# Performance work log

Hardware: AMD Instinct MI355X
Metric: run time of the kernel (lower is better)

The kernel has to match this reference:

```python
import jax, jax.numpy as jnp
import numpy as np

B, L, H, A = 2, 1024, 768, 12          # batch, doc_len, hidden, attn heads
E, M, P = 24, 8, 552                   # entities/doc, mentions/entity, entity pairs/doc
EMB, BLK, NL = 768, 64, 97             # emb_size, block_size, num relation labels
OFFSET = 1                             # [CLS] offset


def setup_inputs() -> dict:
    key = jax.random.key(0)
    ks = jax.random.split(key, 16)
    w = lambda k, shape: (jax.random.normal(k, shape, jnp.float32) * 0.02)
    return {
        'sequence_output': jax.random.normal(ks[0], (B, L, H), jnp.float32),
        'attention': jax.random.uniform(ks[1], (B, A, L, L), jnp.float32),
        'mention_mask': jnp.ones((B, E, M), jnp.float32),
        'Wh': w(ks[2], (2 * H, EMB)),  'bh': jnp.zeros((EMB,), jnp.float32),
        'Wt': w(ks[3], (2 * H, EMB)),  'bt': jnp.zeros((EMB,), jnp.float32),
        'Wh2': w(ks[4], (3 * H, EMB)), 'bh2': jnp.zeros((EMB,), jnp.float32),
        'Wt2': w(ks[5], (3 * H, EMB)), 'bt2': jnp.zeros((EMB,), jnp.float32),
        'W2': w(ks[6], (EMB * BLK, H)), 'b2': jnp.zeros((H,), jnp.float32),
        'Wb': w(ks[7], (EMB * BLK, NL)), 'bb': jnp.zeros((NL,), jnp.float32),
        'mention_idx': jax.random.randint(ks[8], (B, E, M), 0, L - OFFSET),
        'hts': jax.random.randint(ks[9], (B, P, 2), 0, E),
    }


def _block_bilinear(a, b):
    # grouped (block) bilinear: [N, EMB] x [N, EMB] -> [N, EMB*BLK]
    b1 = a.reshape(-1, EMB // BLK, BLK)
    b2 = b.reshape(-1, EMB // BLK, BLK)
    return jnp.einsum('nkb,nkc->nkbc', b1, b2).reshape(-1, EMB * BLK)


def reference(sequence_output, attention, mention_mask,
              Wh, bh, Wt, bt, Wh2, bh2, Wt2, bt2, W2, b2, Wb, bb,
              mention_idx, hts):
    bidx = jnp.arange(B)[:, None, None]
    pos = mention_idx + OFFSET                              # [B,E,M]

    # --- get_hrt: ragged mention gather + logsumexp / mean pooling ---
    ment_emb = sequence_output[bidx, pos]                   # [B,E,M,H]
    mm = mention_mask[..., None]
    x = jnp.where(mm > 0, ment_emb, -1e30)
    mx = x.max(axis=2, keepdims=True)
    ent_emb = (mx + jnp.log(jnp.sum(jnp.exp(x - mx), axis=2, keepdims=True))).squeeze(2)  # [B,E,H]

    ment_att = attention[bidx, :, pos]                      # [B,E,M,A,L]
    cnt = jnp.clip(mention_mask.sum(-1), 1.0)[:, :, None, None]
    ent_att = (ment_att * mention_mask[..., None, None]).sum(2) / cnt  # [B,E,A,L]

    bidx2 = jnp.arange(B)[:, None]
    hs = ent_emb[bidx2, hts[..., 0]]                        # [B,P,H]
    ts = ent_emb[bidx2, hts[..., 1]]
    h_att = ent_att[bidx2, hts[..., 0]]                     # [B,P,A,L]
    t_att = ent_att[bidx2, hts[..., 1]]
    ht_att = (h_att * t_att).mean(2)                        # [B,P,L]
    ht_att = ht_att / (ht_att.sum(-1, keepdims=True) + 1e-30)
    rs = jnp.einsum('bpl,blh->bph', ht_att, sequence_output)  # localized context

    hs = hs.reshape(-1, H); ts = ts.reshape(-1, H); rs = rs.reshape(-1, H)

    # --- forward_rel: extractors + grouped block-bilinear scoring ---
    hs1 = jnp.tanh(jnp.concatenate([hs, rs], -1) @ Wh + bh)
    ts1 = jnp.tanh(jnp.concatenate([ts, rs], -1) @ Wt + bt)
    hts_feat = _block_bilinear(hs1, ts1) @ W2 + b2          # [N,H]
    hs2 = jnp.tanh(jnp.concatenate([hs1, rs, hts_feat], -1) @ Wh2 + bh2)
    ts2 = jnp.tanh(jnp.concatenate([ts1, rs, hts_feat], -1) @ Wt2 + bt2)
    logits = _block_bilinear(hs2, ts2) @ Wb + bb            # [N,NL]
    return logits
```

## Files before the change

### kernel.cpp

```cpp
#include <hip/hip_runtime.h>
#include <hip/hip_bf16.h>

#define B_ 2
#define L_ 1024
#define H_ 768
#define A_ 12
#define E_ 24
#define M_ 8
#define P_ 552
#define EMB_ 768
#define BLK_ 64
#define NBLK_ 12
#define NL_ 97
#define NP_ (B_*P_)
#define KTOT_ 49152
#define TP_ 8
#define LC_ 128
#define NC_ (L_/LC_)

typedef float f32x4 __attribute__((ext_vector_type(4)));
typedef _Float16 f16x8 __attribute__((ext_vector_type(8)));

static __device__ __forceinline__ unsigned short f2h(float f){
    _Float16 h = (_Float16)f;
    unsigned short u; __builtin_memcpy(&u, &h, 2); return u;
}

__global__ void k_ent_emb(const float* __restrict__ seq, const float* __restrict__ mask,
                          const int* __restrict__ midx, float* __restrict__ ent_emb)
{
    int be = blockIdx.x;
    int b = be / E_;
    int h = threadIdx.x;
    float v[M_];
    float mx = -1e30f;
    #pragma unroll
    for (int m = 0; m < M_; ++m) {
        float w = mask[be*M_ + m];
        int p = midx[be*M_ + m] + 1;
        float x = (w > 0.f) ? seq[(b*L_ + p)*H_ + h] : -1e30f;
        v[m] = x; mx = fmaxf(mx, x);
    }
    float s = 0.f;
    #pragma unroll
    for (int m = 0; m < M_; ++m) s += expf(v[m] - mx);
    ent_emb[be*H_ + h] = mx + logf(s);
}

__global__ void k_ent_att(const float* __restrict__ att, const float* __restrict__ mask,
                          const int* __restrict__ midx, float* __restrict__ ent_att)
{
    int bea = blockIdx.x;
    int a = bea % A_;
    int be = bea / A_;
    int b = be / E_;
    float cnt = 0.f;
    #pragma unroll
    for (int m = 0; m < M_; ++m) cnt += mask[be*M_ + m];
    cnt = fmaxf(cnt, 1.f);
    float inv = 1.f / cnt;
    for (int l = threadIdx.x; l < L_; l += blockDim.x) {
        float acc = 0.f;
        #pragma unroll
        for (int m = 0; m < M_; ++m) {
            float w = mask[be*M_ + m];
            if (w > 0.f) {
                int p = midx[be*M_ + m] + 1;
                acc += w * att[((size_t)(b*A_ + a)*L_ + p)*L_ + l];
            }
        }
        ent_att[(size_t)(be*A_ + a)*L_ + l] = acc * inv;
    }
}

__global__ void k_ht_att(const float* __restrict__ ent_att, const int* __restrict__ hts,
                         float* __restrict__ ht_att)
{
    int bp = blockIdx.x;
    int b = bp / P_;
    int he = hts[bp*2 + 0];
    int te = hts[bp*2 + 1];
    const float* ha = ent_att + (size_t)(b*E_ + he)*A_*L_;
    const float* ta = ent_att + (size_t)(b*E_ + te)*A_*L_;
    __shared__ float red[256];
    float lsum = 0.f;
    for (int l = threadIdx.x; l < L_; l += 256) {
        float q = 0.f;
        #pragma unroll
        for (int a = 0; a < A_; ++a) q += ha[a*L_ + l] * ta[a*L_ + l];
        q *= (1.f / A_);
        ht_att[(size_t)bp*L_ + l] = q;
        lsum += q;
    }
    red[threadIdx.x] = lsum;
    __syncthreads();
    for (int s = 128; s > 0; s >>= 1) {
        if (threadIdx.x < s) red[threadIdx.x] += red[threadIdx.x + s];
        __syncthreads();
    }
    float scale = 1.f / (red[0] + 1e-30f);
    for (int l = threadIdx.x; l < L_; l += 256)
        ht_att[(size_t)bp*L_ + l] *= scale;
}

__global__ void k_rs_part(const float* __restrict__ seq, const float* __restrict__ ht_att,
                          float* __restrict__ rspart)
{
    int blk = blockIdx.x;
    int chunk = blockIdx.y;
    int b = blk / (P_/TP_);
    int p0 = (blk % (P_/TP_)) * TP_;
    const float* sq = seq + ((size_t)b*L_ + (size_t)chunk*LC_)*H_;
    const float* wb = ht_att + (size_t)(b*P_ + p0)*L_ + chunk*LC_;
    float acc[TP_][3];
    #pragma unroll
    for (int t = 0; t < TP_; ++t)
        #pragma unroll
        for (int c = 0; c < 3; ++c) acc[t][c] = 0.f;
    for (int l = 0; l < LC_; ++l) {
        float w[TP_];
        #pragma unroll
        for (int t = 0; t < TP_; ++t) w[t] = wb[(size_t)t*L_ + l];
        #pragma unroll
        for (int c = 0; c < 3; ++c) {
            float v = sq[(size_t)l*H_ + threadIdx.x + 256*c];
            #pragma unroll
            for (int t = 0; t < TP_; ++t) acc[t][c] += w[t]*v;
        }
    }
    #pragma unroll
    for (int t = 0; t < TP_; ++t)
        #pragma unroll
        for (int c = 0; c < 3; ++c)
            rspart[((size_t)chunk*NP_ + b*P_ + p0 + t)*H_ + threadIdx.x + 256*c] = acc[t][c];
}

__global__ void k_rs_reduce(const float* __restrict__ rspart, float* __restrict__ rs)
{
    int idx = blockIdx.x*256 + threadIdx.x;
    if (idx >= NP_*768/4) return;
    f32x4 s = {0.f,0.f,0.f,0.f};
    #pragma unroll
    for (int z = 0; z < NC_; ++z) s += *(const f32x4*)&rspart[(size_t)z*NP_*768 + (size_t)idx*4];
    *(f32x4*)&rs[(size_t)idx*4] = s;
}

__global__ void k_rs(const float* __restrict__ seq, const float* __restrict__ ht_att,
                     float* __restrict__ rs)
{
    int blk = blockIdx.x;
    int b = blk / (P_/TP_);
    int p0 = (blk % (P_/TP_)) * TP_;
    const float* sq = seq + (size_t)b*L_*H_;
    float acc[TP_][3];
    #pragma unroll
    for (int t = 0; t < TP_; ++t)
        #pragma unroll
        for (int c = 0; c < 3; ++c) acc[t][c] = 0.f;
    for (int l = 0; l < L_; ++l) {
        float w[TP_];
        #pragma unroll
        for (int t = 0; t < TP_; ++t) w[t] = ht_att[(size_t)(b*P_ + p0 + t)*L_ + l];
        #pragma unroll
        for (int c = 0; c < 3; ++c) {
            float v = sq[(size_t)l*H_ + threadIdx.x + 256*c];
            #pragma unroll
            for (int t = 0; t < TP_; ++t) acc[t][c] += w[t]*v;
        }
    }
    #pragma unroll
    for (int t = 0; t < TP_; ++t)
        #pragma unroll
        for (int c = 0; c < 3; ++c)
            rs[(size_t)(b*P_ + p0 + t)*H_ + threadIdx.x + 256*c] = acc[t][c];
}

__global__ void k_gather(const float* __restrict__ ent_emb, const int* __restrict__ hts,
                         float* __restrict__ hs, float* __restrict__ ts)
{
    int bp = blockIdx.x;
    int b = bp / P_;
    int he = hts[bp*2 + 0];
    int te = hts[bp*2 + 1];
    int h = threadIdx.x;
    hs[(size_t)bp*H_ + h] = ent_emb[(b*E_ + he)*H_ + h];
    ts[(size_t)bp*H_ + h] = ent_emb[(b*E_ + te)*H_ + h];
}

__global__ void k_gemm_reduce_tanh2(const float* __restrict__ gpA, const float* __restrict__ gpB,
                                    const float* __restrict__ biasA, const float* __restrict__ biasB,
                                    float* __restrict__ CA, float* __restrict__ CB, int nz)
{
    const float* Cpart = blockIdx.y ? gpB : gpA;
    const float* bias  = blockIdx.y ? biasB : biasA;
    float* C           = blockIdx.y ? CB : CA;
    int idx = blockIdx.x*256 + threadIdx.x;
    if (idx >= NP_*768/4) return;
    int c4 = (idx*4) % 768;
    f32x4 s = *(const f32x4*)&bias[c4];
    for (int z = 0; z < nz; ++z) s += *(const f32x4*)&Cpart[(size_t)z*NP_*768 + (size_t)idx*4];
    f32x4 r;
    #pragma unroll
    for (int j = 0; j < 4; ++j) r[j] = tanhf(s[j]);
    *(f32x4*)&C[(size_t)idx*4] = r;
}

template<int NPARTS, bool DOTANH>
__global__ void k_gemm_concat(const float* __restrict__ A0, const float* __restrict__ A1,
                              const float* __restrict__ A2, const float* __restrict__ W,
                              const float* __restrict__ bias, float* __restrict__ C,
                              int Mrows)
{
    const int BK = 16;
    __shared__ float As[BK][64];
    __shared__ float Bs[BK][64];
    int tid = threadIdx.x;
    int ty = tid >> 4, tx = tid & 15;
    int by = blockIdx.y, bx = blockIdx.x;
    float acc[4][4] = {};
    const int K = NPARTS * 768;
    for (int kk0 = 0; kk0 < K; kk0 += BK) {
        const float* Ap = (kk0 < 768) ? A0 : ((NPARTS >= 3 && kk0 >= 1536) ? A2 : A1);
        int klocal = kk0 % 768;
        {
            int idx = tid * 4;
            int r = idx >> 4;
            int k = idx & 15;
            int row = by*64 + r;
            float4 v = make_float4(0.f,0.f,0.f,0.f);
            if (row < Mrows) v = *(const float4*)(Ap + (size_t)row*768 + klocal + k);
            As[k+0][r] = v.x; As[k+1][r] = v.y; As[k+2][r] = v.z; As[k+3][r] = v.w;
        }
        {
            int idx = tid * 4;
            int k = idx >> 6;
            int c = idx & 63;
            *(float4*)&Bs[k][c] = *(const float4*)(W + (size_t)(kk0 + k)*768 + bx*64 + c);
        }
        __syncthreads();
        #pragma unroll
        for (int k = 0; k < BK; ++k) {
            float a4[4], b4[4];
            *(float4*)a4 = *(float4*)&As[k][ty*4];
            *(float4*)b4 = *(float4*)&Bs[k][tx*4];
            #pragma unroll
            for (int i = 0; i < 4; ++i)
                #pragma unroll
                for (int j = 0; j < 4; ++j) acc[i][j] += a4[i]*b4[j];
        }
        __syncthreads();
    }
    #pragma unroll
    for (int i = 0; i < 4; ++i) {
        int row = by*64 + ty*4 + i;
        if (row >= Mrows) continue;
        #pragma unroll
        for (int j = 0; j < 4; ++j) {
            int col = bx*64 + tx*4 + j;
            float v = acc[i][j] + bias[col];
            if (DOTANH) v = tanhf(v);
            C[(size_t)row*768 + col] = v;
        }
    }
}

__global__ void k_wt_f16(const float* __restrict__ in, unsigned short* __restrict__ out,
                         int K, int N, int Npad)
{
    __shared__ float t[64][65];
    int k0 = blockIdx.x*64, c0 = blockIdx.y*64;
    int tx = threadIdx.x & 63, ty = threadIdx.x >> 6;
    #pragma unroll
    for (int q = 0; q < 16; ++q) {
        int r = ty*16 + q;
        float v = 0.f;
        if (c0 + tx < N) v = in[(size_t)(k0 + r)*N + c0 + tx];
        t[r][tx] = v;
    }
    __syncthreads();
    #pragma unroll
    for (int q = 0; q < 16; ++q) {
        int col = ty*16 + q;
        if (c0 + col < Npad) out[(size_t)(c0+col)*K + k0 + tx] = f2h(t[tx][col]);
    }
}

__global__ void k_wt_f16x2(const float* __restrict__ in0, unsigned short* __restrict__ out0,
                           const float* __restrict__ in1, unsigned short* __restrict__ out1,
                           int K, int N, int Npad)
{
    const float* in = blockIdx.z ? in1 : in0;
    unsigned short* out = blockIdx.z ? out1 : out0;
    __shared__ float t[64][65];
    int k0 = blockIdx.x*64, c0 = blockIdx.y*64;
    int tx = threadIdx.x & 63, ty = threadIdx.x >> 6;
    #pragma unroll
    for (int q = 0; q < 16; ++q) {
        int r = ty*16 + q;
        float v = 0.f;
        if (c0 + tx < N) v = in[(size_t)(k0 + r)*N + c0 + tx];
        t[r][tx] = v;
    }
    __syncthreads();
    #pragma unroll
    for (int q = 0; q < 16; ++q) {
        int col = ty*16 + q;
        if (c0 + col < Npad) out[(size_t)(c0+col)*K + k0 + tx] = f2h(t[tx][col]);
    }
}

template<int NSTEP>
__launch_bounds__(256, 3)
__global__ void k_gemm_mfma2(const float* __restrict__ A0a, const float* __restrict__ A0b,
                             const float* __restrict__ A1, const float* __restrict__ A2,
                             const unsigned short* __restrict__ WTa, const unsigned short* __restrict__ WTb,
                             float* __restrict__ Cpa, float* __restrict__ Cpb,
                             int Mrows, int Ktot, int partdiv, int nzhalf)
{
    __shared__ _Float16 Ash[128][64];
    __shared__ _Float16 Bsh[128][64];
    int tid = threadIdx.x;
    int lane = tid & 63, wid = tid >> 6;
    int wr = (wid >> 1)*64, wc = (wid & 1)*64;
    int r16 = lane & 15, g = lane >> 4;
    int zz = blockIdx.z;
    int half = zz / nzhalf;
    int z = zz % nzhalf;
    const unsigned short* WT = half ? WTb : WTa;
    float* Cpart = half ? Cpb : Cpa;
    int part = z / partdiv, chunk = z % partdiv;
    int ka = chunk * (NSTEP*64);
    int kb = part*768 + ka;
    const float* A = (part == 0) ? (half ? A0b : A0a) : ((part == 1) ? A1 : A2);
    int c0 = blockIdx.x*128;
    int row0 = blockIdx.y*128;

    f32x4 acc[4][4];
    #pragma unroll
    for (int a = 0; a < 4; ++a)
        #pragma unroll
        for (int b = 0; b < 4; ++b) acc[a][b] = (f32x4){0.f,0.f,0.f,0.f};

    for (int s = 0; s < NSTEP; ++s) {
        __syncthreads();
        #pragma unroll
        for (int q = 0; q < 4; ++q) {
            int idx = q*256 + tid;
            int row = idx >> 3, ch = idx & 7;
            int grow = row0 + row; if (grow >= Mrows) grow = Mrows - 1;
            const float* p = &A[(size_t)grow*768 + ka + s*64 + ch*8];
            f32x4 a0 = *(const f32x4*)p;
            f32x4 a1 = *(const f32x4*)(p + 4);
            f16x8 h;
            h[0]=(_Float16)a0[0]; h[1]=(_Float16)a0[1]; h[2]=(_Float16)a0[2]; h[3]=(_Float16)a0[3];
            h[4]=(_Float16)a1[0]; h[5]=(_Float16)a1[1]; h[6]=(_Float16)a1[2]; h[7]=(_Float16)a1[3];
            *(f16x8*)&Ash[row][(ch ^ (row & 7))*8] = h;
        }
        #pragma unroll
        for (int q = 0; q < 4; ++q) {
            int idx = q*256 + tid;
            int col = idx >> 3, ch = idx & 7;
            *(f16x8*)&Bsh[col][(ch ^ (col & 7))*8] =
                *(const f16x8*)&WT[(size_t)(c0+col)*Ktot + kb + s*64 + ch*8];
        }
        __syncthreads();
        #pragma unroll
        for (int kk = 0; kk < 2; ++kk) {
            f16x8 bfr[4];
            #pragma unroll
            for (int ni = 0; ni < 4; ++ni)
                bfr[ni] = *(f16x8*)&Bsh[wc + ni*16 + r16][((kk*4 + g) ^ (r16 & 7))*8];
            #pragma unroll
            for (int mi = 0; mi < 4; ++mi) {
                f16x8 afr = *(f16x8*)&Ash[wr + mi*16 + r16][((kk*4 + g) ^ (r16 & 7))*8];
                #pragma unroll
                for (int ni = 0; ni < 4; ++ni)
                    acc[mi][ni] = __builtin_amdgcn_mfma_f32_16x16x32_f16(afr, bfr[ni], acc[mi][ni], 0, 0, 0);
            }
        }
    }

    #pragma unroll
    for (int mi = 0; mi < 4; ++mi)
      #pragma unroll
      for (int ni = 0; ni < 4; ++ni)
        #pragma unroll
        for (int r = 0; r < 4; ++r) {
            int row = row0 + wr + mi*16 + g*4 + r;
            if (row < Mrows)
                Cpart[((size_t)z*Mrows + row)*768 + c0 + wc + ni*16 + r16] = acc[mi][ni][r];
        }
}

template<int ILEN, bool SWZ>
__launch_bounds__(256, 3)
__global__ void k_bb_mfma(const float* __restrict__ U, const float* __restrict__ V,
                          const unsigned short* __restrict__ BT, float* __restrict__ Cpart,
                          int Mrows, int ldc)
{
    const int ISPLIT = 64 / ILEN;
    __shared__ unsigned short Ush[128][ILEN + 2];
    __shared__ _Float16 Bs[2][128][64];
    int tid = threadIdx.x;
    int lane = tid & 63, wid = tid >> 6;
    int wr = (wid >> 1)*64, wc = (wid & 1)*64;
    int r16 = lane & 15, g = lane >> 4;
    int bx = blockIdx.x, by = blockIdx.y, z = blockIdx.z;
    if (SWZ) {
        int h = bx + 6*by + 54*z;
        int x = h & 7, j = h >> 3;
        int p = x*9 + j/9;
        by = j % 9;
        bx = p % 6;
        z  = p / 6;
    }
    int kz = z / ISPLIT, si = z % ISPLIT;
    int ibeg = si * ILEN;
    int c0 = bx*128;
    int row0 = by*128;

    #pragma unroll
    for (int q = 0; q < (128*ILEN)/1024; ++q) {
        int idx = (q*256 + tid)*4;
        int r = idx / ILEN, c = idx % ILEN;
        int row = row0 + r; if (row >= Mrows) row = Mrows - 1;
        f32x4 v = *(const f32x4*)&U[(size_t)row*EMB_ + kz*64 + ibeg + c];
        Ush[r][c+0] = f2h(v[0]); Ush[r][c+1] = f2h(v[1]);
        Ush[r][c+2] = f2h(v[2]); Ush[r][c+3] = f2h(v[3]);
    }
    f16x8 vfh[2][4];
    #pragma unroll
    for (int kk = 0; kk < 2; ++kk)
      #pragma unroll
      for (int mi = 0; mi < 4; ++mi) {
        int row = row0 + wr + mi*16 + r16; if (row >= Mrows) row = Mrows - 1;
        const float* p = &V[(size_t)row*EMB_ + kz*64 + kk*32 + g*8];
        f16x8 t;
        #pragma unroll
        for (int e = 0; e < 8; ++e) t[e] = (_Float16)p[e];
        vfh[kk][mi] = t;
      }
    #pragma unroll
    for (int q = 0; q < 4; ++q) {
        int idx = q*256 + tid;
        int col = idx >> 3, ch = idx & 7;
        *(f16x8*)&Bs[0][col][(ch ^ (col & 7))*8] =
            *(const f16x8*)&BT[(size_t)(c0+col)*KTOT_ + (size_t)kz*4096 + (size_t)ibeg*64 + ch*8];
    }
    __syncthreads();

    f32x4 acc[4][4];
    #pragma unroll
    for (int a = 0; a < 4; ++a)
        #pragma unroll
        for (int b = 0; b < 4; ++b) acc[a][b] = (f32x4){0.f,0.f,0.f,0.f};

    f16x8 breg[4];
    for (int ii = 0; ii < ILEN; ++ii) {
        int cur = ii & 1, nxt = cur ^ 1;
        if (ii < ILEN-1) {
            #pragma unroll
            for (int q = 0; q < 4; ++q) {
                int idx = q*256 + tid;
                int col = idx >> 3, ch = idx & 7;
                breg[q] = *(const f16x8*)&BT[(size_t)(c0+col)*KTOT_ + (size_t)kz*4096
                                             + (size_t)(ibeg+ii+1)*64 + ch*8];
            }
        }
        f16x8 u8[4];
        #pragma unroll
        for (int mi = 0; mi < 4; ++mi) {
            unsigned short ub = Ush[wr + mi*16 + r16][ii];
            _Float16 uh; __builtin_memcpy(&uh, &ub, 2);
            #pragma unroll
            for (int e = 0; e < 8; ++e) u8[mi][e] = uh;
        }
        #pragma unroll
        for (int kk = 0; kk < 2; ++kk) {
            f16x8 bfr[4];
            #pragma unroll
            for (int ni = 0; ni < 4; ++ni) {
                int row = wc + ni*16 + r16;
                bfr[ni] = *(f16x8*)&Bs[cur][row][((kk*4 + g) ^ (r16 & 7))*8];
            }
            #pragma unroll
            for (int mi = 0; mi < 4; ++mi) {
                f16x8 afr = u8[mi] * vfh[kk][mi];
                #pragma unroll
                for (int ni = 0; ni < 4; ++ni)
                    acc[mi][ni] = __builtin_amdgcn_mfma_f32_16x16x32_f16(afr, bfr[ni], acc[mi][ni], 0, 0, 0);
            }
        }
        if (ii < ILEN-1) {
            #pragma unroll
            for (int q = 0; q < 4; ++q) {
                int idx = q*256 + tid;
                int col = idx >> 3, ch = idx & 7;
                *(f16x8*)&Bs[nxt][col][(ch ^ (col & 7))*8] = breg[q];
            }
        }
        __syncthreads();
    }

    #pragma unroll
    for (int mi = 0; mi < 4; ++mi)
      #pragma unroll
      for (int ni = 0; ni < 4; ++ni)
        #pragma unroll
        for (int r = 0; r < 4; ++r) {
            int row = row0 + wr + mi*16 + g*4 + r;
            if (row < Mrows)
                Cpart[((size_t)z*Mrows + row)*ldc + c0 + wc + ni*16 + r16] = acc[mi][ni][r];
        }
}

__global__ void k_reduce_feat(const float* __restrict__ part, const float* __restrict__ bias,
                              float* __restrict__ out)
{
    int idx = blockIdx.x*256 + threadIdx.x;
    if (idx >= (NP_*768)/4) return;
    int c4 = (idx*4) % 768;
    f32x4 s = *(const f32x4*)&bias[c4];
    #pragma unroll
    for (int z = 0; z < NBLK_; ++z) s += *(const f32x4*)&part[(size_t)z*NP_*768 + (size_t)idx*4];
    *(f32x4*)&out[(size_t)idx*4] = s;
}

__global__ void k_reduce_logits(const float* __restrict__ part, const float* __restrict__ bb,
                                float* __restrict__ out, int nz)
{
    int idx = blockIdx.x*256 + threadIdx.x;
    if (idx >= NP_*NL_) return;
    int n = idx / NL_, c = idx % NL_;
    float s = bb[c];
    for (int z = 0; z < nz; ++z) s += part[(size_t)z*NP_*128 + (size_t)n*128 + c];
    out[idx] = s;
}

template<bool GUARD, bool SPLITK>
__global__ void k_bbgemm(const float* __restrict__ U, const float* __restrict__ V,
                         const float* __restrict__ W, const float* __restrict__ bias,
                         float* __restrict__ C, int Mrows, int Ncols, int ldw, int ldc)
{
    __shared__ float Us[64][68];
    __shared__ float Vs[64][68];
    __shared__ float Bsh[16][64];
    int tid = threadIdx.x;
    int ty = tid >> 4, tx = tid & 15;
    int by = blockIdx.y, bx = blockIdx.x;
    int c0 = bx*64;
    float acc[4][4] = {};
    int kbeg = SPLITK ? blockIdx.z : 0;
    int kend = SPLITK ? blockIdx.z + 1 : NBLK_;
    for (int k = kbeg; k < kend; ++k) {
        #pragma unroll
        for (int e = 0; e < 4; ++e) {
            int idx = (e*256 + tid)*4;
            int r = idx >> 6, c = idx & 63;
            int row = by*64 + r;
            float4 u = make_float4(0.f,0.f,0.f,0.f), vv = make_float4(0.f,0.f,0.f,0.f);
            if (row < Mrows) {
                u  = *(const float4*)(U + (size_t)row*EMB_ + k*BLK_ + c);
                vv = *(const float4*)(V + (size_t)row*EMB_ + k*BLK_ + c);
            }
            *(float4*)&Us[r][c] = u;
            *(float4*)&Vs[r][c] = vv;
        }
        __syncthreads();
        for (int t = 0; t < 256; ++t) {
            int i = t >> 2;
            int jb = (t & 3) * 16;
            {
                int idx = tid * 4;
                int kk = idx >> 6, c = idx & 63;
                size_t wrow = (size_t)(k*256 + t)*16 + kk;
                if (GUARD) {
                    #pragma unroll
                    for (int q = 0; q < 4; ++q) {
                        int col = c0 + c + q;
                        Bsh[kk][c+q] = (col < Ncols) ? W[wrow*ldw + col] : 0.f;
                    }
                } else {
                    *(float4*)&Bsh[kk][c] = *(const float4*)(W + wrow*ldw + c0 + c);
                }
            }
            __syncthreads();
            float u[4];
            #pragma unroll
            for (int r = 0; r < 4; ++r) u[r] = Us[ty*4+r][i];
            #pragma unroll
            for (int kk = 0; kk < 16; ++kk) {
                float b4[4];
                *(float4*)b4 = *(float4*)&Bsh[kk][tx*4];
                #pragma unroll
                for (int r = 0; r < 4; ++r) {
                    float a = u[r] * Vs[ty*4+r][jb+kk];
                    #pragma unroll
                    for (int j = 0; j < 4; ++j) acc[r][j] += a*b4[j];
                }
            }
            __syncthreads();
        }
    }
    #pragma unroll
    for (int r = 0; r < 4; ++r) {
        int row = by*64 + ty*4 + r;
        if (row >= Mrows) continue;
        #pragma unroll
        for (int j = 0; j < 4; ++j) {
            int col = c0 + tx*4 + j;
            if (GUARD && col >= Ncols) continue;
            float v = acc[r][j];
            if (!SPLITK) v += bias[col];
            size_t out_idx = SPLITK ? ((size_t)(blockIdx.z*Mrows + row)*ldc + col)
                                    : ((size_t)row*ldc + col);
            C[out_idx] = v;
        }
    }
}

__global__ void k_logits_reduce_old(const float* __restrict__ part, const float* __restrict__ bb,
                                    float* __restrict__ out)
{
    int idx = blockIdx.x*256 + threadIdx.x;
    if (idx >= NP_*NL_) return;
    int col = idx % NL_;
    float s = bb[col];
    #pragma unroll
    for (int z = 0; z < NBLK_; ++z) s += part[(size_t)z*NP_*NL_ + idx];
    out[idx] = s;
}

extern "C" void kernel_launch(void* const* d_in, const int* in_sizes, int n_in,
                              void* d_out, int out_size, void* d_ws, size_t ws_size,
                              hipStream_t stream)
{
    (void)in_sizes; (void)n_in; (void)out_size;
    const float* seq  = (const float*)d_in[0];
    const float* att  = (const float*)d_in[1];
    const float* mask = (const float*)d_in[2];
    const float* Wh   = (const float*)d_in[3];
    const float* bh   = (const float*)d_in[4];
    const float* Wt   = (const float*)d_in[5];
    const float* bt   = (const float*)d_in[6];
    const float* Wh2  = (const float*)d_in[7];
    const float* bh2  = (const float*)d_in[8];
    const float* Wt2  = (const float*)d_in[9];
    const float* bt2  = (const float*)d_in[10];
    const float* W2   = (const float*)d_in[11];
    const float* b2   = (const float*)d_in[12];
    const float* Wb   = (const float*)d_in[13];
    const float* bb   = (const float*)d_in[14];
    const int* midx   = (const int*)d_in[15];
    const int* hts    = (const int*)d_in[16];
    float* out = (float*)d_out;
    float* ws  = (float*)d_ws;

    float* ent_emb = ws;
    float* ent_att = ent_emb + 36864;
    float* ht_att  = ent_att + 589824;
    float* rs      = ht_att + 1130496;
    float* hs      = rs   + 847872;
    float* ts      = hs   + 847872;
    float* hs1     = ts   + 847872;
    float* ts1     = hs1  + 847872;
    float* feat    = ts1  + 847872;
    float* hs2     = feat + 847872;
    float* ts2     = hs2  + 847872;
    float* featpart = ts2 + 847872;
    float* spare    = featpart + 10174464;
    unsigned short* w2t = (unsigned short*)(spare + 1695744);
    unsigned short* Rrgn = (unsigned short*)(spare + 1695744 + 18874368);
    const size_t need_bytes = (size_t)42430464 * 4;
    const bool use_mfma = (ws_size >= need_bytes);

    unsigned short* whT  = Rrgn;
    unsigned short* wtT  = Rrgn + 1179648;
    unsigned short* wh2T = Rrgn;
    unsigned short* wt2T = Rrgn + 1769472;
    unsigned short* wbt  = Rrgn;

    float* rspart  = featpart;
    float* gpA     = featpart;
    float* gpB     = featpart + 5087232;
    float* logpart = featpart;

    k_ent_emb<<<dim3(B_*E_), dim3(H_), 0, stream>>>(seq, mask, midx, ent_emb);
    k_ent_att<<<dim3(B_*E_*A_), dim3(256), 0, stream>>>(att, mask, midx, ent_att);
    k_ht_att<<<dim3(NP_), dim3(256), 0, stream>>>(ent_att, hts, ht_att);

    if (use_mfma) {
        k_rs_part<<<dim3(B_*(P_/TP_), NC_), dim3(256), 0, stream>>>(seq, ht_att, rspart);
        k_rs_reduce<<<dim3(828), dim3(256), 0, stream>>>(rspart, rs);
        k_gather<<<dim3(NP_), dim3(H_), 0, stream>>>(ent_emb, hts, hs, ts);

        k_wt_f16x2<<<dim3(1536/64, 768/64, 2), dim3(256), 0, stream>>>(Wh, whT, Wt, wtT, 1536, 768, 768);

        k_gemm_mfma2<4><<<dim3(6, 9, 12), dim3(256), 0, stream>>>(
            hs, ts, rs, rs, whT, wtT, gpA, gpB, NP_, 1536, 3, 6);
        k_gemm_reduce_tanh2<<<dim3(828, 2), dim3(256), 0, stream>>>(gpA, gpB, bh, bt, hs1, ts1, 6);

        k_wt_f16<<<dim3(KTOT_/64, 768/64), dim3(256), 0, stream>>>(W2, w2t, KTOT_, 768, 768);
        k_bb_mfma<64, true><<<dim3(6, 9, NBLK_), dim3(256), 0, stream>>>(hs1, ts1, w2t, featpart, NP_, 768);
        k_reduce_feat<<<dim3((NP_*768/4 + 255)/256), dim3(256), 0, stream>>>(featpart, b2, feat);

        k_wt_f16x2<<<dim3(2304/64, 768/64, 2), dim3(256), 0, stream>>>(Wh2, wh2T, Wt2, wt2T, 2304, 768, 768);

        k_gemm_mfma2<6><<<dim3(6, 9, 12), dim3(256), 0, stream>>>(
            hs1, ts1, rs, feat, wh2T, wt2T, gpA, gpB, NP_, 2304, 2, 6);
        k_gemm_reduce_tanh2<<<dim3(828, 2), dim3(256), 0, stream>>>(gpA, gpB, bh2, bt2, hs2, ts2, 6);

        k_wt_f16<<<dim3(KTOT_/64, 128/64), dim3(256), 0, stream>>>(Wb, wbt, KTOT_, NL_, 128);
        k_bb_mfma<16, false><<<dim3(1, 9, NBLK_*4), dim3(256), 0, stream>>>(hs2, ts2, wbt, logpart, NP_, 128);
        k_reduce_logits<<<dim3((NP_*NL_ + 255)/256), dim3(256), 0, stream>>>(logpart, bb, out, NBLK_*4);
    } else {
        k_rs<<<dim3(B_*(P_/TP_)), dim3(256), 0, stream>>>(seq, ht_att, rs);
        k_gather<<<dim3(NP_), dim3(H_), 0, stream>>>(ent_emb, hts, hs, ts);
        dim3 gg(12, (NP_+63)/64);
        k_gemm_concat<2, true><<<gg, dim3(256), 0, stream>>>(hs, rs, nullptr, Wh, bh, hs1, NP_);
        k_gemm_concat<2, true><<<gg, dim3(256), 0, stream>>>(ts, rs, nullptr, Wt, bt, ts1, NP_);
        float* lpart = featpart;
        k_bbgemm<false, false><<<gg, dim3(256), 0, stream>>>(hs1, ts1, W2, b2, feat, NP_, 768, 768, 768);
        k_gemm_concat<3, true><<<gg, dim3(256), 0, stream>>>(hs1, rs, feat, Wh2, bh2, hs2, NP_);
        k_gemm_concat<3, true><<<gg, dim3(256), 0, stream>>>(ts1, rs, feat, Wt2, bt2, ts2, NP_);
        k_bbgemm<true, true><<<dim3(2, (NP_+63)/64, NBLK_), dim3(256), 0, stream>>>(
            hs2, ts2, Wb, nullptr, lpart, NP_, NL_, NL_, NL_);
        k_logits_reduce_old<<<dim3((NP_*NL_ + 255)/256), dim3(256), 0, stream>>>(lpart, bb, out);
    }
}
```

Before: 392.9 us.

## Compute localized context with MFMA GEMM and fuse gather into extractor GEMM

Replaces the scalar FP32 rs_part kernel with an MFMA f16 GEMM over ht_att and a transposed f16 copy of sequence_output. The transpose is merged with the W2 conversion into one multi-task transpose kernel. The hs/ts gather kernel is removed: the first extractor GEMM indexes ent_emb directly through hts. This cuts launches and scalar FMA work, at the cost of f16 rounding of the attention weights and the sequence values in the rs computation.

Result: faster. 349.5 us (-11.0%).

```diff
diff --git a/kernel.cpp b/kernel.cpp
--- a/kernel.cpp
+++ b/kernel.cpp
@@ -15,8 +15,7 @@
 #define NP_ (B_*P_)
 #define KTOT_ 49152
 #define TP_ 8
-#define LC_ 128
-#define NC_ (L_/LC_)
+#define NC_ 8
 
 typedef float f32x4 __attribute__((ext_vector_type(4)));
 typedef _Float16 f16x8 __attribute__((ext_vector_type(8)));
@@ -103,36 +102,147 @@
         ht_att[(size_t)bp*L_ + l] *= scale;
 }
 
-__global__ void k_rs_part(const float* __restrict__ seq, const float* __restrict__ ht_att,
-                          float* __restrict__ rspart)
-{
-    int blk = blockIdx.x;
-    int chunk = blockIdx.y;
-    int b = blk / (P_/TP_);
-    int p0 = (blk % (P_/TP_)) * TP_;
-    const float* sq = seq + ((size_t)b*L_ + (size_t)chunk*LC_)*H_;
-    const float* wb = ht_att + (size_t)(b*P_ + p0)*L_ + chunk*LC_;
-    float acc[TP_][3];
-    #pragma unroll
-    for (int t = 0; t < TP_; ++t)
-        #pragma unroll
-        for (int c = 0; c < 3; ++c) acc[t][c] = 0.f;
-    for (int l = 0; l < LC_; ++l) {
-        float w[TP_];
-        #pragma unroll
-        for (int t = 0; t < TP_; ++t) w[t] = wb[(size_t)t*L_ + l];
-        #pragma unroll
-        for (int c = 0; c < 3; ++c) {
-            float v = sq[(size_t)l*H_ + threadIdx.x + 256*c];
-            #pragma unroll
-            for (int t = 0; t < TP_; ++t) acc[t][c] += w[t]*v;
-        }
-    }
-    #pragma unroll
-    for (int t = 0; t < TP_; ++t)
-        #pragma unroll
-        for (int c = 0; c < 3; ++c)
-            rspart[((size_t)chunk*NP_ + b*P_ + p0 + t)*H_ + threadIdx.x + 256*c] = acc[t][c];
+__global__ void k_wt_multi(const float* __restrict__ W2, unsigned short* __restrict__ w2t,
+                           const float* __restrict__ seq, unsigned short* __restrict__ seqT)
+{
+    int t = blockIdx.x;
+    const float* in; unsigned short* out; int K, N, kt, ct;
+    if (t < 9216)       { in = W2;              out = w2t;             K = KTOT_; N = 768; kt = t % 768; ct = t / 768; }
+    else if (t < 9408)  { t -= 9216; in = seq;                 out = seqT;              K = L_; N = 768; kt = t % 16; ct = t / 16; }
+    else                { t -= 9408; in = seq + (size_t)L_*H_; out = seqT + (size_t)768*L_; K = L_; N = 768; kt = t % 16; ct = t / 16; }
+    __shared__ float tl[64][65];
+    int k0 = kt*64, c0 = ct*64;
+    int tx = threadIdx.x & 63, ty = threadIdx.x >> 6;
+    #pragma unroll
+    for (int q = 0; q < 16; ++q) {
+        int r = ty*16 + q;
+        tl[r][tx] = in[(size_t)(k0 + r)*N + c0 + tx];
+    }
+    __syncthreads();
+    #pragma unroll
+    for (int q = 0; q < 16; ++q) {
+        int col = ty*16 + q;
+        out[(size_t)(c0+col)*K + k0 + tx] = f2h(tl[tx][col]);
+    }
+}
+
+__global__ void k_wt_f16(const float* __restrict__ in, unsigned short* __restrict__ out,
+                         int K, int N, int Npad)
+{
+    __shared__ float t[64][65];
+    int k0 = blockIdx.x*64, c0 = blockIdx.y*64;
+    int tx = threadIdx.x & 63, ty = threadIdx.x >> 6;
+    #pragma unroll
+    for (int q = 0; q < 16; ++q) {
+        int r = ty*16 + q;
+        float v = 0.f;
+        if (c0 + tx < N) v = in[(size_t)(k0 + r)*N + c0 + tx];
+        t[r][tx] = v;
+    }
+    __syncthreads();
+    #pragma unroll
+    for (int q = 0; q < 16; ++q) {
+        int col = ty*16 + q;
+        if (c0 + col < Npad) out[(size_t)(c0+col)*K + k0 + tx] = f2h(t[tx][col]);
+    }
+}
+
+__global__ void k_wt_f16x2(const float* __restrict__ in0, unsigned short* __restrict__ out0,
+                           const float* __restrict__ in1, unsigned short* __restrict__ out1,
+                           int K, int N, int Npad)
+{
+    const float* in = blockIdx.z ? in1 : in0;
+    unsigned short* out = blockIdx.z ? out1 : out0;
+    __shared__ float t[64][65];
+    int k0 = blockIdx.x*64, c0 = blockIdx.y*64;
+    int tx = threadIdx.x & 63, ty = threadIdx.x >> 6;
+    #pragma unroll
+    for (int q = 0; q < 16; ++q) {
+        int r = ty*16 + q;
+        float v = 0.f;
+        if (c0 + tx < N) v = in[(size_t)(k0 + r)*N + c0 + tx];
+        t[r][tx] = v;
+    }
+    __syncthreads();
+    #pragma unroll
+    for (int q = 0; q < 16; ++q) {
+        int col = ty*16 + q;
+        if (c0 + col < Npad) out[(size_t)(c0+col)*K + k0 + tx] = f2h(t[tx][col]);
+    }
+}
+
+__launch_bounds__(256, 3)
+__global__ void k_rs_mfma(const float* __restrict__ ht_att, const unsigned short* __restrict__ seqT,
+                          float* __restrict__ Cpart)
+{
+    __shared__ _Float16 Ash[128][64];
+    __shared__ _Float16 Bsh[128][64];
+    int tid = threadIdx.x;
+    int lane = tid & 63, wid = tid >> 6;
+    int wr = (wid >> 1)*64, wc = (wid & 1)*64;
+    int r16 = lane & 15, g = lane >> 4;
+    int z = blockIdx.z;
+    int b = z >> 3, kc = z & 7;
+    int c0 = blockIdx.x*128;
+    int row0 = blockIdx.y*128;
+    const float* At = ht_att + (size_t)b*P_*L_;
+    const unsigned short* Bt = seqT + (size_t)b*768*L_;
+
+    f32x4 acc[4][4];
+    #pragma unroll
+    for (int a = 0; a < 4; ++a)
+        #pragma unroll
+        for (int bq = 0; bq < 4; ++bq) acc[a][bq] = (f32x4){0.f,0.f,0.f,0.f};
+
+    for (int s = 0; s < 2; ++s) {
+        __syncthreads();
+        #pragma unroll
+        for (int q = 0; q < 4; ++q) {
+            int idx = q*256 + tid;
+            int row = idx >> 3, ch = idx & 7;
+            int p = row0 + row; if (p >= P_) p = P_ - 1;
+            const float* pp = &At[(size_t)p*L_ + kc*128 + s*64 + ch*8];
+            f32x4 a0 = *(const f32x4*)pp;
+            f32x4 a1 = *(const f32x4*)(pp + 4);
+            f16x8 h;
+            h[0]=(_Float16)a0[0]; h[1]=(_Float16)a0[1]; h[2]=(_Float16)a0[2]; h[3]=(_Float16)a0[3];
+            h[4]=(_Float16)a1[0]; h[5]=(_Float16)a1[1]; h[6]=(_Float16)a1[2]; h[7]=(_Float16)a1[3];
+            *(f16x8*)&Ash[row][(ch ^ (row & 7))*8] = h;
+        }
+        #pragma unroll
+        for (int q = 0; q < 4; ++q) {
+            int idx = q*256 + tid;
+            int col = idx >> 3, ch = idx & 7;
+            *(f16x8*)&Bsh[col][(ch ^ (col & 7))*8] =
+                *(const f16x8*)&Bt[(size_t)(c0+col)*L_ + kc*128 + s*64 + ch*8];
+        }
+        __syncthreads();
+        #pragma unroll
+        for (int kk = 0; kk < 2; ++kk) {
+            f16x8 bfr[4];
+            #pragma unroll
+            for (int ni = 0; ni < 4; ++ni)
+                bfr[ni] = *(f16x8*)&Bsh[wc + ni*16 + r16][((kk*4 + g) ^ (r16 & 7))*8];
+            #pragma unroll
+            for (int mi = 0; mi < 4; ++mi) {
+                f16x8 afr = *(f16x8*)&Ash[wr + mi*16 + r16][((kk*4 + g) ^ (r16 & 7))*8];
+                #pragma unroll
+                for (int ni = 0; ni < 4; ++ni)
+                    acc[mi][ni] = __builtin_amdgcn_mfma_f32_16x16x32_f16(afr, bfr[ni], acc[mi][ni], 0, 0, 0);
+            }
+        }
+    }
+
+    #pragma unroll
+    for (int mi = 0; mi < 4; ++mi)
+      #pragma unroll
+      for (int ni = 0; ni < 4; ++ni)
+        #pragma unroll
+        for (int r = 0; r < 4; ++r) {
+            int p = row0 + wr + mi*16 + g*4 + r;
+            if (p < P_)
+                Cpart[((size_t)kc*NP_ + b*P_ + p)*768 + c0 + wc + ni*16 + r16] = acc[mi][ni][r];
+        }
 }
 
 __global__ void k_rs_reduce(const float* __restrict__ rspart, float* __restrict__ rs)
@@ -264,55 +374,11 @@
     }
 }
 
-__global__ void k_wt_f16(const float* __restrict__ in, unsigned short* __restrict__ out,
-                         int K, int N, int Npad)
-{
-    __shared__ float t[64][65];
-    int k0 = blockIdx.x*64, c0 = blockIdx.y*64;
-    int tx = threadIdx.x & 63, ty = threadIdx.x >> 6;
-    #pragma unroll
-    for (int q = 0; q < 16; ++q) {
-        int r = ty*16 + q;
-        float v = 0.f;
-        if (c0 + tx < N) v = in[(size_t)(k0 + r)*N + c0 + tx];
-        t[r][tx] = v;
-    }
-    __syncthreads();
-    #pragma unroll
-    for (int q = 0; q < 16; ++q) {
-        int col = ty*16 + q;
-        if (c0 + col < Npad) out[(size_t)(c0+col)*K + k0 + tx] = f2h(t[tx][col]);
-    }
-}
-
-__global__ void k_wt_f16x2(const float* __restrict__ in0, unsigned short* __restrict__ out0,
-                           const float* __restrict__ in1, unsigned short* __restrict__ out1,
-                           int K, int N, int Npad)
-{
-    const float* in = blockIdx.z ? in1 : in0;
-    unsigned short* out = blockIdx.z ? out1 : out0;
-    __shared__ float t[64][65];
-    int k0 = blockIdx.x*64, c0 = blockIdx.y*64;
-    int tx = threadIdx.x & 63, ty = threadIdx.x >> 6;
-    #pragma unroll
-    for (int q = 0; q < 16; ++q) {
-        int r = ty*16 + q;
-        float v = 0.f;
-        if (c0 + tx < N) v = in[(size_t)(k0 + r)*N + c0 + tx];
-        t[r][tx] = v;
-    }
-    __syncthreads();
-    #pragma unroll
-    for (int q = 0; q < 16; ++q) {
-        int col = ty*16 + q;
-        if (c0 + col < Npad) out[(size_t)(c0+col)*K + k0 + tx] = f2h(t[tx][col]);
-    }
-}
-
-template<int NSTEP>
+template<int NSTEP, bool GATHER0>
 __launch_bounds__(256, 3)
 __global__ void k_gemm_mfma2(const float* __restrict__ A0a, const float* __restrict__ A0b,
                              const float* __restrict__ A1, const float* __restrict__ A2,
+                             const int* __restrict__ hts,
                              const unsigned short* __restrict__ WTa, const unsigned short* __restrict__ WTb,
                              float* __restrict__ Cpa, float* __restrict__ Cpb,
                              int Mrows, int Ktot, int partdiv, int nzhalf)
@@ -348,7 +414,14 @@
             int idx = q*256 + tid;
             int row = idx >> 3, ch = idx & 7;
             int grow = row0 + row; if (grow >= Mrows) grow = Mrows - 1;
-            const float* p = &A[(size_t)grow*768 + ka + s*64 + ch*8];
+            const float* p;
+            if (GATHER0 && part == 0) {
+                int bb_ = grow / P_;
+                int e = hts[grow*2 + half];
+                p = &A0a[((size_t)(bb_*E_ + e))*768 + ka + s*64 + ch*8];
+            } else {
+                p = &A[(size_t)grow*768 + ka + s*64 + ch*8];
+            }
             f32x4 a0 = *(const f32x4*)p;
             f32x4 a1 = *(const f32x4*)(p + 4);
             f16x8 h;
@@ -680,6 +753,8 @@
     unsigned short* wt2T = Rrgn + 1769472;
     unsigned short* wbt  = Rrgn;
 
+    unsigned short* seqT = (unsigned short*)hs;
+
     float* rspart  = featpart;
     float* gpA     = featpart;
     float* gpB     = featpart + 5087232;
@@ -690,24 +765,24 @@
     k_ht_att<<<dim3(NP_), dim3(256), 0, stream>>>(ent_att, hts, ht_att);
 
     if (use_mfma) {
-        k_rs_part<<<dim3(B_*(P_/TP_), NC_), dim3(256), 0, stream>>>(seq, ht_att, rspart);
+        k_wt_multi<<<dim3(9600), dim3(256), 0, stream>>>(W2, w2t, seq, seqT);
+
+        k_rs_mfma<<<dim3(6, 5, 16), dim3(256), 0, stream>>>(ht_att, seqT, rspart);
         k_rs_reduce<<<dim3(828), dim3(256), 0, stream>>>(rspart, rs);
-        k_gather<<<dim3(NP_), dim3(H_), 0, stream>>>(ent_emb, hts, hs, ts);
 
         k_wt_f16x2<<<dim3(1536/64, 768/64, 2), dim3(256), 0, stream>>>(Wh, whT, Wt, wtT, 1536, 768, 768);
 
-        k_gemm_mfma2<4><<<dim3(6, 9, 12), dim3(256), 0, stream>>>(
-            hs, ts, rs, rs, whT, wtT, gpA, gpB, NP_, 1536, 3, 6);
+        k_gemm_mfma2<4, true><<<dim3(6, 9, 12), dim3(256), 0, stream>>>(
+            ent_emb, ent_emb, rs, rs, hts, whT, wtT, gpA, gpB, NP_, 1536, 3, 6);
         k_gemm_reduce_tanh2<<<dim3(828, 2), dim3(256), 0, stream>>>(gpA, gpB, bh, bt, hs1, ts1, 6);
 
-        k_wt_f16<<<dim3(KTOT_/64, 768/64), dim3(256), 0, stream>>>(W2, w2t, KTOT_, 768, 768);
         k_bb_mfma<64, true><<<dim3(6, 9, NBLK_), dim3(256), 0, stream>>>(hs1, ts1, w2t, featpart, NP_, 768);
         k_reduce_feat<<<dim3((NP_*768/4 + 255)/256), dim3(256), 0, stream>>>(featpart, b2, feat);
 
         k_wt_f16x2<<<dim3(2304/64, 768/64, 2), dim3(256), 0, stream>>>(Wh2, wh2T, Wt2, wt2T, 2304, 768, 768);
 
-        k_gemm_mfma2<6><<<dim3(6, 9, 12), dim3(256), 0, stream>>>(
-            hs1, ts1, rs, feat, wh2T, wt2T, gpA, gpB, NP_, 2304, 2, 6);
+        k_gemm_mfma2<6, false><<<dim3(6, 9, 12), dim3(256), 0, stream>>>(
+            hs1, ts1, rs, feat, hts, wh2T, wt2T, gpA, gpB, NP_, 2304, 2, 6);
         k_gemm_reduce_tanh2<<<dim3(828, 2), dim3(256), 0, stream>>>(gpA, gpB, bh2, bt2, hs2, ts2, 6);
 
         k_wt_f16<<<dim3(KTOT_/64, 128/64), dim3(256), 0, stream>>>(Wb, wbt, KTOT_, NL_, 128);
```
